# Optimization experiments

Measured on AMD Instinct MI355X. Metric: run time of the kernel, lower is better.

Reference implementation:

```python
import jax, jax.numpy as jnp
import numpy as np

B, S, F, E, R, O = 4, 2048, 2048, 16, 16, 2048
TEMPERATURE = 1.0


def setup_inputs() -> dict:
    key = jax.random.key(0)
    k1, k2, k3, k4 = jax.random.split(key, 4)
    x = jax.random.normal(k1, (B, S, F), dtype=jnp.float32)
    prototypes = jax.random.normal(k2, (E, F), dtype=jnp.float32)
    # prototypes are top right-singular vectors -> unit norm rows
    prototypes = prototypes / jnp.linalg.norm(prototypes, axis=1, keepdims=True)
    A_stack = jax.random.normal(k3, (E, R, F), dtype=jnp.float32) * 0.02
    B_stack = jax.random.normal(k4, (E, O, R), dtype=jnp.float32) * 0.02
    scaling = jnp.float32(2.0)
    return {"x": x, "prototypes": prototypes, "A_stack": A_stack,
            "B_stack": B_stack, "scaling": scaling, "top_k": 4}


def reference(x, prototypes, A_stack, B_stack, scaling, top_k):
    lead = x.shape[:-1]
    f_in = x.shape[-1]
    tok = x.reshape(-1, f_in)                       # (t, F)
    t = tok.shape[0]

    # Arrow routing: abs cosine-like similarity to per-expert prototypes
    sim = jnp.abs(tok @ prototypes.T)               # (t, E)
    top_v, idx = jax.lax.top_k(sim, top_k)          # (t, k)
    full_score = jnp.full(sim.shape, -jnp.inf, dtype=sim.dtype)
    full_score = full_score.at[jnp.arange(t)[:, None], idx].set(top_v)
    coeff = jax.nn.softmax(full_score / TEMPERATURE, axis=1)  # (t, E), zeros off top-k

    # Per-expert LoRA: z = tok @ A_e^T  (dense over all experts, as in source)
    z = jnp.einsum('tf,erf->ter', tok, A_stack)     # (t, E, r)
    # Combine coeff into the low-rank space before the B projection to avoid
    # materializing the (t, E, out) tensor; math identical to
    # einsum('te, teo -> to', coeff, einsum('ter,eor->teo', z, B_stack)).
    delta = jnp.einsum('te,ter,eor->to', coeff, z, B_stack)  # (t, O)

    delta = scaling * delta                          # dropout = identity (eval)
    return delta.reshape(lead + (delta.shape[-1],))
```

## Files before the change

### kernel.cpp

```cpp
#include <hip/hip_runtime.h>
#include <hip/hip_bf16.h>
#include <stdint.h>

#define T_TOKENS 8192
#define F_DIM    2048
#define E_EXP    16
#define R_RANK   16
#define O_DIM    2048
#define KDIM     (E_EXP * R_RANK)

typedef short v8s __attribute__((ext_vector_type(8)));
typedef float v4f __attribute__((ext_vector_type(4)));

#define AS1 __attribute__((address_space(1)))
#define AS3 __attribute__((address_space(3)))

__device__ __forceinline__ uint16_t f2bf(float f) {
  uint32_t u = __builtin_bit_cast(uint32_t, f);
  u += 0x7fffu + ((u >> 16) & 1u);
  return (uint16_t)(u >> 16);
}

__device__ __forceinline__ void g2lds16(const uint16_t* g, uint16_t* l) {
  __builtin_amdgcn_global_load_lds((AS1 void*)g, (AS3 void*)l, 16, 0, 0);
}

__global__ __launch_bounds__(256) void prep_weights(
    const float* __restrict__ A, const float* __restrict__ Bst,
    uint16_t* __restrict__ Ab, uint16_t* __restrict__ Bb) {
  int idx = blockIdx.x * 256 + threadIdx.x;
  if (idx < KDIM * F_DIM) {
    Ab[idx] = f2bf(A[idx]);
  }
  if (idx < O_DIM * KDIM) {
    int k = idx & (KDIM - 1);
    int o = idx >> 8;
    int e = k >> 4, r = k & 15;
    Bb[idx] = f2bf(Bst[((size_t)e * O_DIM + o) * R_RANK + r]);
  }
}

__global__ __launch_bounds__(256) void route_stream(
    const float* __restrict__ x, const float* __restrict__ P,
    uint16_t* __restrict__ xb, float4* __restrict__ partials4) {
  __shared__ float ps[16 * 260];
  const int tid = threadIdx.x;
  const int c   = blockIdx.x;
  const int by  = blockIdx.y;
  const int f0  = c * 256;

  {
    const int e = tid >> 4;
    #pragma unroll
    for (int j = 0; j < 4; ++j) {
      const int col = (tid & 15) * 4 + j * 64;
      *(float4*)&ps[e * 260 + col] =
          *(const float4*)&P[(size_t)e * F_DIM + f0 + col];
    }
  }
  __syncthreads();

  const int sub = tid & 15;
  const int tg  = tid >> 4;
  const int t0  = by * 64 + tg * 4;
  const float* xr = x + (size_t)t0 * F_DIM + f0;
  uint16_t*    xw = xb + (size_t)t0 * F_DIM + f0;

  float a0[16], a1[16], a2[16], a3[16];
  #pragma unroll
  for (int e = 0; e < 16; ++e) { a0[e] = 0.f; a1[e] = 0.f; a2[e] = 0.f; a3[e] = 0.f; }

  #pragma unroll
  for (int j = 0; j < 4; ++j) {
    const int off = sub * 4 + j * 64;
    float4 v0 = *(const float4*)&xr[off];
    float4 v1 = *(const float4*)&xr[F_DIM + off];
    float4 v2 = *(const float4*)&xr[2 * F_DIM + off];
    float4 v3 = *(const float4*)&xr[3 * F_DIM + off];
    uint2 p0, p1, p2, p3;
    p0.x = (uint32_t)f2bf(v0.x) | ((uint32_t)f2bf(v0.y) << 16);
    p0.y = (uint32_t)f2bf(v0.z) | ((uint32_t)f2bf(v0.w) << 16);
    p1.x = (uint32_t)f2bf(v1.x) | ((uint32_t)f2bf(v1.y) << 16);
    p1.y = (uint32_t)f2bf(v1.z) | ((uint32_t)f2bf(v1.w) << 16);
    p2.x = (uint32_t)f2bf(v2.x) | ((uint32_t)f2bf(v2.y) << 16);
    p2.y = (uint32_t)f2bf(v2.z) | ((uint32_t)f2bf(v2.w) << 16);
    p3.x = (uint32_t)f2bf(v3.x) | ((uint32_t)f2bf(v3.y) << 16);
    p3.y = (uint32_t)f2bf(v3.z) | ((uint32_t)f2bf(v3.w) << 16);
    *(uint2*)&xw[off]             = p0;
    *(uint2*)&xw[F_DIM + off]     = p1;
    *(uint2*)&xw[2 * F_DIM + off] = p2;
    *(uint2*)&xw[3 * F_DIM + off] = p3;
    #pragma unroll
    for (int e = 0; e < 16; ++e) {
      float4 pv = *(float4*)&ps[e * 260 + off];
      a0[e] += v0.x * pv.x; a0[e] += v0.y * pv.y; a0[e] += v0.z * pv.z; a0[e] += v0.w * pv.w;
      a1[e] += v1.x * pv.x; a1[e] += v1.y * pv.y; a1[e] += v1.z * pv.z; a1[e] += v1.w * pv.w;
      a2[e] += v2.x * pv.x; a2[e] += v2.y * pv.y; a2[e] += v2.z * pv.z; a2[e] += v2.w * pv.w;
      a3[e] += v3.x * pv.x; a3[e] += v3.y * pv.y; a3[e] += v3.z * pv.z; a3[e] += v3.w * pv.w;
    }
  }

  #pragma unroll
  for (int e = 0; e < 16; ++e) {
    #pragma unroll
    for (int m = 1; m < 16; m <<= 1) {
      a0[e] += __shfl_xor(a0[e], m, 64);
      a1[e] += __shfl_xor(a1[e], m, 64);
      a2[e] += __shfl_xor(a2[e], m, 64);
      a3[e] += __shfl_xor(a3[e], m, 64);
    }
  }

  const size_t cb = (size_t)c * 4;
  if (sub == 0) {
    #pragma unroll
    for (int e4 = 0; e4 < 4; ++e4)
      partials4[(cb + e4) * T_TOKENS + t0] =
          make_float4(a0[e4 * 4], a0[e4 * 4 + 1], a0[e4 * 4 + 2], a0[e4 * 4 + 3]);
  } else if (sub == 1) {
    #pragma unroll
    for (int e4 = 0; e4 < 4; ++e4)
      partials4[(cb + e4) * T_TOKENS + t0 + 1] =
          make_float4(a1[e4 * 4], a1[e4 * 4 + 1], a1[e4 * 4 + 2], a1[e4 * 4 + 3]);
  } else if (sub == 2) {
    #pragma unroll
    for (int e4 = 0; e4 < 4; ++e4)
      partials4[(cb + e4) * T_TOKENS + t0 + 2] =
          make_float4(a2[e4 * 4], a2[e4 * 4 + 1], a2[e4 * 4 + 2], a2[e4 * 4 + 3]);
  } else if (sub == 3) {
    #pragma unroll
    for (int e4 = 0; e4 < 4; ++e4)
      partials4[(cb + e4) * T_TOKENS + t0 + 3] =
          make_float4(a3[e4 * 4], a3[e4 * 4 + 1], a3[e4 * 4 + 2], a3[e4 * 4 + 3]);
  }
}

__global__ __launch_bounds__(256) void gemm_xa(
    const uint16_t* __restrict__ xb, const uint16_t* __restrict__ Ab,
    const float4* __restrict__ partials4, const float* __restrict__ scaling,
    const int* __restrict__ topk, uint16_t* __restrict__ wb) {
  __shared__ uint16_t S[16384];
  __shared__ float coeffL[64 * 17];
  uint16_t* Xh[2] = { S,         S + 4096  };
  uint16_t* Ah[2] = { S + 8192,  S + 12288 };
  const int tid  = threadIdx.x;
  const int b    = blockIdx.x;
  const int m_idx = (b & 7) + ((b >> 5) << 3);
  const int n_idx = (b >> 3) & 3;
  const int m0 = m_idx * 64, n0 = n_idx * 64;
  const int lane = tid & 63;
  const int wid  = tid >> 6;
  const int wm   = (wid >> 1) * 32;
  const int wn   = (wid & 1) * 32;
  const int quad = lane >> 4;
  const int cl   = lane & 15;

  if (tid < 64) {
    const int t = m0 + tid;
    double s[16];
    #pragma unroll
    for (int e = 0; e < 16; ++e) s[e] = 0.0;
    for (int c = 0; c < 8; ++c) {
      #pragma unroll
      for (int e4 = 0; e4 < 4; ++e4) {
        float4 p = partials4[((size_t)c * 4 + e4) * T_TOKENS + t];
        s[e4 * 4]     += (double)p.x;
        s[e4 * 4 + 1] += (double)p.y;
        s[e4 * 4 + 2] += (double)p.z;
        s[e4 * 4 + 3] += (double)p.w;
      }
    }
    double v[16];
    #pragma unroll
    for (int e = 0; e < 16; ++e) v[e] = fabs(s[e]);
    int k = topk[0];
    if (k > 16) k = 16;
    if (k < 1)  k = 1;
    unsigned mask = 0;
    double mx = 0.0;
    float ssum = 0.f;
    for (int i = 0; i < k; ++i) {
      double bv = -1.0; int bj = 0;
      #pragma unroll
      for (int j = 0; j < 16; ++j) {
        bool ok = !((mask >> j) & 1u) && (v[j] > bv);
        bv = ok ? v[j] : bv;
        bj = ok ? j  : bj;
      }
      mask |= 1u << bj;
      if (i == 0) mx = bv;
      ssum += expf((float)(bv - mx));
    }
    const float sc = scaling[0];
    #pragma unroll
    for (int j = 0; j < 16; ++j)
      coeffL[tid * 17 + j] = ((mask >> j) & 1u)
          ? expf((float)(v[j] - mx)) / ssum * sc : 0.f;
  }

  const int G0 = wid * 64 + lane;
  const int G1 = G0 + 256;
  const int r0 = G0 >> 3, g0 = (G0 & 7) ^ (r0 & 7);
  const int r1 = G1 >> 3, g1 = (G1 & 7) ^ (r1 & 7);
  const uint16_t* xs0 = xb + (size_t)(m0 + r0) * F_DIM + g0 * 8;
  const uint16_t* xs1 = xb + (size_t)(m0 + r1) * F_DIM + g1 * 8;
  const uint16_t* as0 = Ab + (size_t)(n0 + r0) * F_DIM + g0 * 8;
  const uint16_t* as1 = Ab + (size_t)(n0 + r1) * F_DIM + g1 * 8;
  const int d0 = wid * 512;
  const int d1 = wid * 512 + 2048;

  const int ma0 = wm + cl, ma1 = wm + 16 + cl;
  const int nb0 = wn + cl, nb1 = wn + 16 + cl;

  v4f acc[2][2];
  #pragma unroll
  for (int i = 0; i < 2; i++)
    #pragma unroll
    for (int j = 0; j < 2; j++) acc[i][j] = (v4f){0.f, 0.f, 0.f, 0.f};

  for (int k0 = 0; k0 < F_DIM; k0 += 128) {
    __syncthreads();
    g2lds16(xs0 + k0,      Xh[0] + d0);
    g2lds16(xs1 + k0,      Xh[0] + d1);
    g2lds16(as0 + k0,      Ah[0] + d0);
    g2lds16(as1 + k0,      Ah[0] + d1);
    g2lds16(xs0 + k0 + 64, Xh[1] + d0);
    g2lds16(xs1 + k0 + 64, Xh[1] + d1);
    g2lds16(as0 + k0 + 64, Ah[1] + d0);
    g2lds16(as1 + k0 + 64, Ah[1] + d1);
    __syncthreads();
    #pragma unroll
    for (int h = 0; h < 2; ++h) {
      #pragma unroll
      for (int ks = 0; ks < 2; ++ks) {
        const int gk = ks * 4 + quad;
        v8s fa0 = *(v8s*)&Xh[h][(ma0 * 8 + (gk ^ (ma0 & 7))) * 8];
        v8s fa1 = *(v8s*)&Xh[h][(ma1 * 8 + (gk ^ (ma1 & 7))) * 8];
        v8s fb0 = *(v8s*)&Ah[h][(nb0 * 8 + (gk ^ (nb0 & 7))) * 8];
        v8s fb1 = *(v8s*)&Ah[h][(nb1 * 8 + (gk ^ (nb1 & 7))) * 8];
        acc[0][0] = __builtin_amdgcn_mfma_f32_16x16x32_bf16(fa0, fb0, acc[0][0], 0, 0, 0);
        acc[0][1] = __builtin_amdgcn_mfma_f32_16x16x32_bf16(fa0, fb1, acc[0][1], 0, 0, 0);
        acc[1][0] = __builtin_amdgcn_mfma_f32_16x16x32_bf16(fa1, fb0, acc[1][0], 0, 0, 0);
        acc[1][1] = __builtin_amdgcn_mfma_f32_16x16x32_bf16(fa1, fb1, acc[1][1], 0, 0, 0);
      }
    }
  }

  __syncthreads();
  uint16_t* tile = S;
  #pragma unroll
  for (int mi = 0; mi < 2; mi++)
    #pragma unroll
    for (int ni = 0; ni < 2; ni++) {
      const int nl = wn + ni * 16 + cl;
      const int eidx = (n0 + nl) >> 4;
      #pragma unroll
      for (int reg = 0; reg < 4; reg++) {
        const int tl = wm + mi * 16 + quad * 4 + reg;
        float wv = acc[mi][ni][reg] * coeffL[tl * 17 + eidx];
        tile[tl * 72 + nl] = f2bf(wv);
      }
    }
  __syncthreads();
  #pragma unroll
  for (int p = 0; p < 2; ++p) {
    const int row  = p * 32 + (tid >> 3);
    const int colg = (tid & 7) * 8;
    uint4 val = *(uint4*)&tile[row * 72 + colg];
    *(uint4*)&wb[(size_t)(m0 + row) * KDIM + n0 + colg] = val;
  }
}

__global__ __launch_bounds__(256) void gemm_wb(
    const uint16_t* __restrict__ wbuf, const uint16_t* __restrict__ Bb,
    float* __restrict__ out) {
  __shared__ uint16_t S[20480];
  uint16_t* Ws = S;
  uint16_t* Bs = S + 4096;
  const int tid  = threadIdx.x;
  const int b    = blockIdx.x;
  const int m_idx = (b & 7) + ((b >> 6) << 3);
  const int n_idx = (b >> 3) & 7;
  const int m0 = m_idx * 64;
  const int n0 = n_idx * 256;
  const int lane = tid & 63;
  const int wid  = tid >> 6;
  const int wm   = (wid >> 1) * 32;
  const int wn   = (wid & 1) * 128;
  const int quad = lane >> 4;
  const int cl   = lane & 15;

  const int GW0 = wid * 64 + lane;
  const int GW1 = GW0 + 256;
  const int wr0 = GW0 >> 3, wg0 = (GW0 & 7) ^ (wr0 & 7);
  const int wr1 = GW1 >> 3, wg1 = (GW1 & 7) ^ (wr1 & 7);
  const uint16_t* wsrc0 = wbuf + (size_t)(m0 + wr0) * KDIM + wg0 * 8;
  const uint16_t* wsrc1 = wbuf + (size_t)(m0 + wr1) * KDIM + wg1 * 8;

  const uint16_t* bsrc[8];
  #pragma unroll
  for (int p = 0; p < 8; ++p) {
    const int G = p * 256 + wid * 64 + lane;
    const int r = G >> 3, g = (G & 7) ^ (r & 7);
    bsrc[p] = Bb + (size_t)(n0 + r) * KDIM + g * 8;
  }

  v4f acc[2][8];
  #pragma unroll
  for (int i = 0; i < 2; i++)
    #pragma unroll
    for (int j = 0; j < 8; j++) acc[i][j] = (v4f){0.f, 0.f, 0.f, 0.f};

  const int ma0 = wm + cl, ma1 = wm + 16 + cl;

  #pragma unroll
  for (int k0 = 0; k0 < KDIM; k0 += 64) {
    __syncthreads();
    g2lds16(wsrc0 + k0, Ws + wid * 512);
    g2lds16(wsrc1 + k0, Ws + wid * 512 + 2048);
    #pragma unroll
    for (int p = 0; p < 8; ++p)
      g2lds16(bsrc[p] + k0, Bs + (p * 256 + wid * 64) * 8);
    __syncthreads();
    #pragma unroll
    for (int ks = 0; ks < 2; ++ks) {
      const int gk = ks * 4 + quad;
      v8s fa0 = *(v8s*)&Ws[(ma0 * 8 + (gk ^ (ma0 & 7))) * 8];
      v8s fa1 = *(v8s*)&Ws[(ma1 * 8 + (gk ^ (ma1 & 7))) * 8];
      v8s fb[8];
      #pragma unroll
      for (int j = 0; j < 8; ++j) {
        const int nb = wn + j * 16 + cl;
        fb[j] = *(v8s*)&Bs[(nb * 8 + (gk ^ (nb & 7))) * 8];
      }
      #pragma unroll
      for (int j = 0; j < 8; ++j) {
        acc[0][j] = __builtin_amdgcn_mfma_f32_16x16x32_bf16(fa0, fb[j], acc[0][j], 0, 0, 0);
        acc[1][j] = __builtin_amdgcn_mfma_f32_16x16x32_bf16(fa1, fb[j], acc[1][j], 0, 0, 0);
      }
    }
  }

  float* ft = (float*)S;
  #pragma unroll
  for (int h = 0; h < 2; ++h) {
    __syncthreads();
    if ((wid >> 1) == h) {
      #pragma unroll
      for (int mi = 0; mi < 2; mi++)
        #pragma unroll
        for (int j = 0; j < 8; j++) {
          const int col = wn + j * 16 + cl;
          #pragma unroll
          for (int reg = 0; reg < 4; reg++) {
            const int rl = mi * 16 + quad * 4 + reg;
            ft[rl * 260 + col] = acc[mi][j][reg];
          }
        }
    }
    __syncthreads();
    #pragma unroll
    for (int p = 0; p < 8; ++p) {
      const int f4  = p * 256 + tid;
      const int row = f4 >> 6;
      const int c4  = f4 & 63;
      float4 v = *(float4*)&ft[row * 260 + c4 * 4];
      *(float4*)&out[(size_t)(m0 + h * 32 + row) * O_DIM + n0 + c4 * 4] = v;
    }
  }
}

extern "C" void kernel_launch(void* const* d_in, const int* in_sizes, int n_in,
                              void* d_out, int out_size, void* d_ws, size_t ws_size,
                              hipStream_t stream) {
  (void)in_sizes; (void)n_in; (void)out_size; (void)ws_size;
  const float* x       = (const float*)d_in[0];
  const float* P       = (const float*)d_in[1];
  const float* A       = (const float*)d_in[2];
  const float* Bst     = (const float*)d_in[3];
  const float* scaling = (const float*)d_in[4];
  const int*   topk    = (const int*)d_in[5];
  float* out = (float*)d_out;

  char* ws = (char*)d_ws;
  uint16_t* xb     = (uint16_t*)(ws);
  uint16_t* Ab     = (uint16_t*)(ws + 33554432);
  uint16_t* Bb     = (uint16_t*)(ws + 34603008);
  uint16_t* wbuf   = (uint16_t*)(ws + 35651584);
  float4*   parts  = (float4*)  (ws + 39845888);

  hipLaunchKernelGGL(prep_weights, dim3(2048), dim3(256), 0, stream, A, Bst, Ab, Bb);
  hipLaunchKernelGGL(route_stream, dim3(8, 128), dim3(256), 0, stream, x, P, xb, parts);
  hipLaunchKernelGGL(gemm_xa, dim3(512), dim3(256), 0, stream,
                     xb, Ab, parts, scaling, topk, wbuf);
  hipLaunchKernelGGL(gemm_wb, dim3(1024), dim3(256), 0, stream, wbuf, Bb, out);
}
```

Before: 167.0 us.

## Fuse weight prep into routing kernel and double-buffer XA GEMM loads

Removes the separate prep_weights launch by appending 64 extra blocks to route_stream that convert A and B to bf16. In gemm_xa, the coefficient computation now runs after the first LDS stage is issued, so its latency overlaps the load. The K loop becomes ping-pong double buffered so the next half-tile is fetched while the current one is multiplied. The aim is to cut launch overhead and hide global-to-LDS latency. The risks are that the few extra conversion blocks run as a tail in route_stream, and that synchronisation between stages becomes more intricate.

```diff
diff --git a/kernel.cpp b/kernel.cpp
--- a/kernel.cpp
+++ b/kernel.cpp
@@ -25,30 +25,30 @@
   __builtin_amdgcn_global_load_lds((AS1 void*)g, (AS3 void*)l, 16, 0, 0);
 }
 
-__global__ __launch_bounds__(256) void prep_weights(
-    const float* __restrict__ A, const float* __restrict__ Bst,
-    uint16_t* __restrict__ Ab, uint16_t* __restrict__ Bb) {
-  int idx = blockIdx.x * 256 + threadIdx.x;
-  if (idx < KDIM * F_DIM) {
-    Ab[idx] = f2bf(A[idx]);
-  }
-  if (idx < O_DIM * KDIM) {
-    int k = idx & (KDIM - 1);
-    int o = idx >> 8;
-    int e = k >> 4, r = k & 15;
-    Bb[idx] = f2bf(Bst[((size_t)e * O_DIM + o) * R_RANK + r]);
-  }
-}
-
 __global__ __launch_bounds__(256) void route_stream(
     const float* __restrict__ x, const float* __restrict__ P,
-    uint16_t* __restrict__ xb, float4* __restrict__ partials4) {
+    const float* __restrict__ A, const float* __restrict__ Bst,
+    uint16_t* __restrict__ xb, float4* __restrict__ partials4,
+    uint16_t* __restrict__ Ab, uint16_t* __restrict__ Bb) {
   __shared__ float ps[16 * 260];
   const int tid = threadIdx.x;
   const int c   = blockIdx.x;
   const int by  = blockIdx.y;
-  const int f0  = c * 256;
-
+
+  if (by >= 128) {
+    const int gid = ((by - 128) * 8 + c) * 256 + tid;
+    for (int i = gid; i < KDIM * F_DIM; i += 64 * 256)
+      Ab[i] = f2bf(A[i]);
+    for (int i = gid; i < O_DIM * KDIM; i += 64 * 256) {
+      const int k = i & (KDIM - 1);
+      const int o = i >> 8;
+      const int e = k >> 4, r = k & 15;
+      Bb[i] = f2bf(Bst[((size_t)e * O_DIM + o) * R_RANK + r]);
+    }
+    return;
+  }
+
+  const int f0 = c * 256;
   {
     const int e = tid >> 4;
     #pragma unroll
@@ -141,8 +141,10 @@
     const int* __restrict__ topk, uint16_t* __restrict__ wb) {
   __shared__ uint16_t S[16384];
   __shared__ float coeffL[64 * 17];
-  uint16_t* Xh[2] = { S,         S + 4096  };
-  uint16_t* Ah[2] = { S + 8192,  S + 12288 };
+  uint16_t* X0 = S;
+  uint16_t* X1 = S + 4096;
+  uint16_t* A0 = S + 8192;
+  uint16_t* A1 = S + 12288;
   const int tid  = threadIdx.x;
   const int b    = blockIdx.x;
   const int m_idx = (b & 7) + ((b >> 5) << 3);
@@ -155,49 +157,6 @@
   const int quad = lane >> 4;
   const int cl   = lane & 15;
 
-  if (tid < 64) {
-    const int t = m0 + tid;
-    double s[16];
-    #pragma unroll
-    for (int e = 0; e < 16; ++e) s[e] = 0.0;
-    for (int c = 0; c < 8; ++c) {
-      #pragma unroll
-      for (int e4 = 0; e4 < 4; ++e4) {
-        float4 p = partials4[((size_t)c * 4 + e4) * T_TOKENS + t];
-        s[e4 * 4]     += (double)p.x;
-        s[e4 * 4 + 1] += (double)p.y;
-        s[e4 * 4 + 2] += (double)p.z;
-        s[e4 * 4 + 3] += (double)p.w;
-      }
-    }
-    double v[16];
-    #pragma unroll
-    for (int e = 0; e < 16; ++e) v[e] = fabs(s[e]);
-    int k = topk[0];
-    if (k > 16) k = 16;
-    if (k < 1)  k = 1;
-    unsigned mask = 0;
-    double mx = 0.0;
-    float ssum = 0.f;
-    for (int i = 0; i < k; ++i) {
-      double bv = -1.0; int bj = 0;
-      #pragma unroll
-      for (int j = 0; j < 16; ++j) {
-        bool ok = !((mask >> j) & 1u) && (v[j] > bv);
-        bv = ok ? v[j] : bv;
-        bj = ok ? j  : bj;
-      }
-      mask |= 1u << bj;
-      if (i == 0) mx = bv;
-      ssum += expf((float)(bv - mx));
-    }
-    const float sc = scaling[0];
-    #pragma unroll
-    for (int j = 0; j < 16; ++j)
-      coeffL[tid * 17 + j] = ((mask >> j) & 1u)
-          ? expf((float)(v[j] - mx)) / ssum * sc : 0.f;
-  }
-
   const int G0 = wid * 64 + lane;
   const int G1 = G0 + 256;
   const int r0 = G0 >> 3, g0 = (G0 & 7) ^ (r0 & 7);
@@ -212,38 +171,86 @@
   const int ma0 = wm + cl, ma1 = wm + 16 + cl;
   const int nb0 = wn + cl, nb1 = wn + 16 + cl;
 
+#define STAGE_XA(Xb_, Ab_, kk) do {       \
+    g2lds16(xs0 + (kk), (Xb_) + d0);      \
+    g2lds16(xs1 + (kk), (Xb_) + d1);      \
+    g2lds16(as0 + (kk), (Ab_) + d0);      \
+    g2lds16(as1 + (kk), (Ab_) + d1);      \
+  } while (0)
+
+#define COMP_XA(Xb_, Ab_) do {                                                            \
+    _Pragma("unroll")                                                                     \
+    for (int ks = 0; ks < 2; ++ks) {                                                      \
+      const int gk = ks * 4 + quad;                                                       \
+      v8s fa0 = *(v8s*)&(Xb_)[(ma0 * 8 + (gk ^ (ma0 & 7))) * 8];                          \
+      v8s fa1 = *(v8s*)&(Xb_)[(ma1 * 8 + (gk ^ (ma1 & 7))) * 8];                          \
+      v8s fb0 = *(v8s*)&(Ab_)[(nb0 * 8 + (gk ^ (nb0 & 7))) * 8];                          \
+      v8s fb1 = *(v8s*)&(Ab_)[(nb1 * 8 + (gk ^ (nb1 & 7))) * 8];                          \
+      acc[0][0] = __builtin_amdgcn_mfma_f32_16x16x32_bf16(fa0, fb0, acc[0][0], 0, 0, 0);  \
+      acc[0][1] = __builtin_amdgcn_mfma_f32_16x16x32_bf16(fa0, fb1, acc[0][1], 0, 0, 0);  \
+      acc[1][0] = __builtin_amdgcn_mfma_f32_16x16x32_bf16(fa1, fb0, acc[1][0], 0, 0, 0);  \
+      acc[1][1] = __builtin_amdgcn_mfma_f32_16x16x32_bf16(fa1, fb1, acc[1][1], 0, 0, 0);  \
+    }                                                                                     \
+  } while (0)
+
   v4f acc[2][2];
   #pragma unroll
   for (int i = 0; i < 2; i++)
     #pragma unroll
     for (int j = 0; j < 2; j++) acc[i][j] = (v4f){0.f, 0.f, 0.f, 0.f};
 
+  STAGE_XA(X0, A0, 0);
+
+  if (tid < 64) {
+    const int t = m0 + tid;
+    double s[16];
+    #pragma unroll
+    for (int e = 0; e < 16; ++e) s[e] = 0.0;
+    for (int c = 0; c < 8; ++c) {
+      #pragma unroll
+      for (int e4 = 0; e4 < 4; ++e4) {
+        float4 p = partials4[((size_t)c * 4 + e4) * T_TOKENS + t];
+        s[e4 * 4]     += (double)p.x;
+        s[e4 * 4 + 1] += (double)p.y;
+        s[e4 * 4 + 2] += (double)p.z;
+        s[e4 * 4 + 3] += (double)p.w;
+      }
+    }
+    double v[16];
+    #pragma unroll
+    for (int e = 0; e < 16; ++e) v[e] = fabs(s[e]);
+    int k = topk[0];
+    if (k > 16) k = 16;
+    if (k < 1)  k = 1;
+    unsigned mask = 0;
+    double mx = 0.0;
+    float ssum = 0.f;
+    for (int i = 0; i < k; ++i) {
+      double bv = -1.0; int bj = 0;
+      #pragma unroll
+      for (int j = 0; j < 16; ++j) {
+        bool ok = !((mask >> j) & 1u) && (v[j] > bv);
+        bv = ok ? v[j] : bv;
+        bj = ok ? j  : bj;
+      }
+      mask |= 1u << bj;
+      if (i == 0) mx = bv;
+      ssum += expf((float)(bv - mx));
+    }
+    const float sc = scaling[0];
+    #pragma unroll
+    for (int j = 0; j < 16; ++j)
+      coeffL[tid * 17 + j] = ((mask >> j) & 1u)
+          ? expf((float)(v[j] - mx)) / ssum * sc : 0.f;
+  }
+
   for (int k0 = 0; k0 < F_DIM; k0 += 128) {
     __syncthreads();
-    g2lds16(xs0 + k0,      Xh[0] + d0);
-    g2lds16(xs1 + k0,      Xh[0] + d1);
-    g2lds16(as0 + k0,      Ah[0] + d0);
-    g2lds16(as1 + k0,      Ah[0] + d1);
-    g2lds16(xs0 + k0 + 64, Xh[1] + d0);
-    g2lds16(xs1 + k0 + 64, Xh[1] + d1);
-    g2lds16(as0 + k0 + 64, Ah[1] + d0);
-    g2lds16(as1 + k0 + 64, Ah[1] + d1);
-    __syncthreads();
-    #pragma unroll
-    for (int h = 0; h < 2; ++h) {
-      #pragma unroll
-      for (int ks = 0; ks < 2; ++ks) {
-        const int gk = ks * 4 + quad;
-        v8s fa0 = *(v8s*)&Xh[h][(ma0 * 8 + (gk ^ (ma0 & 7))) * 8];
-        v8s fa1 = *(v8s*)&Xh[h][(ma1 * 8 + (gk ^ (ma1 & 7))) * 8];
-        v8s fb0 = *(v8s*)&Ah[h][(nb0 * 8 + (gk ^ (nb0 & 7))) * 8];
-        v8s fb1 = *(v8s*)&Ah[h][(nb1 * 8 + (gk ^ (nb1 & 7))) * 8];
-        acc[0][0] = __builtin_amdgcn_mfma_f32_16x16x32_bf16(fa0, fb0, acc[0][0], 0, 0, 0);
-        acc[0][1] = __builtin_amdgcn_mfma_f32_16x16x32_bf16(fa0, fb1, acc[0][1], 0, 0, 0);
-        acc[1][0] = __builtin_amdgcn_mfma_f32_16x16x32_bf16(fa1, fb0, acc[1][0], 0, 0, 0);
-        acc[1][1] = __builtin_amdgcn_mfma_f32_16x16x32_bf16(fa1, fb1, acc[1][1], 0, 0, 0);
-      }
-    }
+    STAGE_XA(X1, A1, k0 + 64);
+    COMP_XA(X0, A0);
+    __syncthreads();
+    if (k0 + 128 < F_DIM) STAGE_XA(X0, A0, k0 + 128);
+    COMP_XA(X1, A1);
   }
 
   __syncthreads();
@@ -269,6 +276,8 @@
     uint4 val = *(uint4*)&tile[row * 72 + colg];
     *(uint4*)&wb[(size_t)(m0 + row) * KDIM + n0 + colg] = val;
   }
+#undef STAGE_XA
+#undef COMP_XA
 }
 
 __global__ __launch_bounds__(256) void gemm_wb(
@@ -389,8 +398,8 @@
   uint16_t* wbuf   = (uint16_t*)(ws + 35651584);
   float4*   parts  = (float4*)  (ws + 39845888);
 
-  hipLaunchKernelGGL(prep_weights, dim3(2048), dim3(256), 0, stream, A, Bst, Ab, Bb);
-  hipLaunchKernelGGL(route_stream, dim3(8, 128), dim3(256), 0, stream, x, P, xb, parts);
+  hipLaunchKernelGGL(route_stream, dim3(8, 136), dim3(256), 0, stream,
+                     x, P, A, Bst, xb, parts, Ab, Bb);
   hipLaunchKernelGGL(gemm_xa, dim3(512), dim3(256), 0, stream,
                      xb, Ab, parts, scaling, topk, wbuf);
   hipLaunchKernelGGL(gemm_wb, dim3(1024), dim3(256), 0, stream, wbuf, Bb, out);
```

Result: slower. 179.5 us (+7.5%).

## Fuse routing, bf16 conversion and x@A GEMM into one LDS-resident kernel

Applied to the files above, without the earlier changes.

Merges the routing/conversion kernel and the x@A GEMM into a single kernel where each block streams 32 token rows of fp32 x, computes prototype similarities, and stores bf16 x in LDS for the MFMA stage. This eliminates the global bf16 copy of x, the partial-sum buffer and one launch. Routing now sums in fp32 instead of double, and the large LDS footprint limits each CU to one block with less latency hiding.

```diff
diff --git a/kernel.cpp b/kernel.cpp
--- a/kernel.cpp
+++ b/kernel.cpp
@@ -21,8 +21,8 @@
   return (uint16_t)(u >> 16);
 }
 
-__device__ __forceinline__ void g2lds16(const uint16_t* g, uint16_t* l) {
-  __builtin_amdgcn_global_load_lds((AS1 void*)g, (AS3 void*)l, 16, 0, 0);
+__device__ __forceinline__ void g2lds16(const void* g, void* l) {
+  __builtin_amdgcn_global_load_lds((const AS1 void*)g, (AS3 void*)l, 16, 0, 0);
 }
 
 __global__ __launch_bounds__(256) void prep_weights(
@@ -40,234 +40,158 @@
   }
 }
 
-__global__ __launch_bounds__(256) void route_stream(
+__global__ __launch_bounds__(256) void fused_xa(
     const float* __restrict__ x, const float* __restrict__ P,
-    uint16_t* __restrict__ xb, float4* __restrict__ partials4) {
-  __shared__ float ps[16 * 260];
-  const int tid = threadIdx.x;
-  const int c   = blockIdx.x;
-  const int by  = blockIdx.y;
-  const int f0  = c * 256;
-
-  {
-    const int e = tid >> 4;
-    #pragma unroll
-    for (int j = 0; j < 4; ++j) {
-      const int col = (tid & 15) * 4 + j * 64;
-      *(float4*)&ps[e * 260 + col] =
-          *(const float4*)&P[(size_t)e * F_DIM + f0 + col];
-    }
-  }
-  __syncthreads();
-
-  const int sub = tid & 15;
-  const int tg  = tid >> 4;
-  const int t0  = by * 64 + tg * 4;
-  const float* xr = x + (size_t)t0 * F_DIM + f0;
-  uint16_t*    xw = xb + (size_t)t0 * F_DIM + f0;
-
-  float a0[16], a1[16], a2[16], a3[16];
-  #pragma unroll
-  for (int e = 0; e < 16; ++e) { a0[e] = 0.f; a1[e] = 0.f; a2[e] = 0.f; a3[e] = 0.f; }
-
-  #pragma unroll
-  for (int j = 0; j < 4; ++j) {
-    const int off = sub * 4 + j * 64;
-    float4 v0 = *(const float4*)&xr[off];
-    float4 v1 = *(const float4*)&xr[F_DIM + off];
-    float4 v2 = *(const float4*)&xr[2 * F_DIM + off];
-    float4 v3 = *(const float4*)&xr[3 * F_DIM + off];
-    uint2 p0, p1, p2, p3;
-    p0.x = (uint32_t)f2bf(v0.x) | ((uint32_t)f2bf(v0.y) << 16);
-    p0.y = (uint32_t)f2bf(v0.z) | ((uint32_t)f2bf(v0.w) << 16);
-    p1.x = (uint32_t)f2bf(v1.x) | ((uint32_t)f2bf(v1.y) << 16);
-    p1.y = (uint32_t)f2bf(v1.z) | ((uint32_t)f2bf(v1.w) << 16);
-    p2.x = (uint32_t)f2bf(v2.x) | ((uint32_t)f2bf(v2.y) << 16);
-    p2.y = (uint32_t)f2bf(v2.z) | ((uint32_t)f2bf(v2.w) << 16);
-    p3.x = (uint32_t)f2bf(v3.x) | ((uint32_t)f2bf(v3.y) << 16);
-    p3.y = (uint32_t)f2bf(v3.z) | ((uint32_t)f2bf(v3.w) << 16);
-    *(uint2*)&xw[off]             = p0;
-    *(uint2*)&xw[F_DIM + off]     = p1;
-    *(uint2*)&xw[2 * F_DIM + off] = p2;
-    *(uint2*)&xw[3 * F_DIM + off] = p3;
-    #pragma unroll
-    for (int e = 0; e < 16; ++e) {
-      float4 pv = *(float4*)&ps[e * 260 + off];
-      a0[e] += v0.x * pv.x; a0[e] += v0.y * pv.y; a0[e] += v0.z * pv.z; a0[e] += v0.w * pv.w;
-      a1[e] += v1.x * pv.x; a1[e] += v1.y * pv.y; a1[e] += v1.z * pv.z; a1[e] += v1.w * pv.w;
-      a2[e] += v2.x * pv.x; a2[e] += v2.y * pv.y; a2[e] += v2.z * pv.z; a2[e] += v2.w * pv.w;
-      a3[e] += v3.x * pv.x; a3[e] += v3.y * pv.y; a3[e] += v3.z * pv.z; a3[e] += v3.w * pv.w;
-    }
-  }
-
-  #pragma unroll
-  for (int e = 0; e < 16; ++e) {
-    #pragma unroll
-    for (int m = 1; m < 16; m <<= 1) {
-      a0[e] += __shfl_xor(a0[e], m, 64);
-      a1[e] += __shfl_xor(a1[e], m, 64);
-      a2[e] += __shfl_xor(a2[e], m, 64);
-      a3[e] += __shfl_xor(a3[e], m, 64);
-    }
-  }
-
-  const size_t cb = (size_t)c * 4;
-  if (sub == 0) {
-    #pragma unroll
-    for (int e4 = 0; e4 < 4; ++e4)
-      partials4[(cb + e4) * T_TOKENS + t0] =
-          make_float4(a0[e4 * 4], a0[e4 * 4 + 1], a0[e4 * 4 + 2], a0[e4 * 4 + 3]);
-  } else if (sub == 1) {
-    #pragma unroll
-    for (int e4 = 0; e4 < 4; ++e4)
-      partials4[(cb + e4) * T_TOKENS + t0 + 1] =
-          make_float4(a1[e4 * 4], a1[e4 * 4 + 1], a1[e4 * 4 + 2], a1[e4 * 4 + 3]);
-  } else if (sub == 2) {
-    #pragma unroll
-    for (int e4 = 0; e4 < 4; ++e4)
-      partials4[(cb + e4) * T_TOKENS + t0 + 2] =
-          make_float4(a2[e4 * 4], a2[e4 * 4 + 1], a2[e4 * 4 + 2], a2[e4 * 4 + 3]);
-  } else if (sub == 3) {
-    #pragma unroll
-    for (int e4 = 0; e4 < 4; ++e4)
-      partials4[(cb + e4) * T_TOKENS + t0 + 3] =
-          make_float4(a3[e4 * 4], a3[e4 * 4 + 1], a3[e4 * 4 + 2], a3[e4 * 4 + 3]);
-  }
-}
-
-__global__ __launch_bounds__(256) void gemm_xa(
-    const uint16_t* __restrict__ xb, const uint16_t* __restrict__ Ab,
-    const float4* __restrict__ partials4, const float* __restrict__ scaling,
+    const uint16_t* __restrict__ Ab, const float* __restrict__ scaling,
     const int* __restrict__ topk, uint16_t* __restrict__ wb) {
-  __shared__ uint16_t S[16384];
-  __shared__ float coeffL[64 * 17];
-  uint16_t* Xh[2] = { S,         S + 4096  };
-  uint16_t* Ah[2] = { S + 8192,  S + 12288 };
+  __shared__ uint16_t SH[75072];
+  uint16_t* xbf   = SH;
+  float*    Pl    = (float*)(SH + 65536);
+  uint16_t* tile  = SH + 65536;
+  float*    coeffL= (float*)((char*)SH + 131072 + 16896);
+
   const int tid  = threadIdx.x;
-  const int b    = blockIdx.x;
-  const int m_idx = (b & 7) + ((b >> 5) << 3);
-  const int n_idx = (b >> 3) & 3;
-  const int m0 = m_idx * 64, n0 = n_idx * 64;
+  const int m0   = blockIdx.x * 32;
   const int lane = tid & 63;
   const int wid  = tid >> 6;
-  const int wm   = (wid >> 1) * 32;
-  const int wn   = (wid & 1) * 32;
   const int quad = lane >> 4;
   const int cl   = lane & 15;
-
-  if (tid < 64) {
-    const int t = m0 + tid;
-    double s[16];
-    #pragma unroll
-    for (int e = 0; e < 16; ++e) s[e] = 0.0;
-    for (int c = 0; c < 8; ++c) {
-      #pragma unroll
-      for (int e4 = 0; e4 < 4; ++e4) {
-        float4 p = partials4[((size_t)c * 4 + e4) * T_TOKENS + t];
-        s[e4 * 4]     += (double)p.x;
-        s[e4 * 4 + 1] += (double)p.y;
-        s[e4 * 4 + 2] += (double)p.z;
-        s[e4 * 4 + 3] += (double)p.w;
-      }
-    }
-    double v[16];
-    #pragma unroll
-    for (int e = 0; e < 16; ++e) v[e] = fabs(s[e]);
-    int k = topk[0];
-    if (k > 16) k = 16;
-    if (k < 1)  k = 1;
-    unsigned mask = 0;
-    double mx = 0.0;
-    float ssum = 0.f;
-    for (int i = 0; i < k; ++i) {
-      double bv = -1.0; int bj = 0;
-      #pragma unroll
-      for (int j = 0; j < 16; ++j) {
-        bool ok = !((mask >> j) & 1u) && (v[j] > bv);
-        bv = ok ? v[j] : bv;
-        bj = ok ? j  : bj;
-      }
-      mask |= 1u << bj;
-      if (i == 0) mx = bv;
-      ssum += expf((float)(bv - mx));
-    }
+  const int tg   = tid >> 4;
+  const int slot = tid & 15;
+
+  float part0[16], part1[16];
+  #pragma unroll
+  for (int e = 0; e < 16; ++e) { part0[e] = 0.f; part1[e] = 0.f; }
+
+  const float* xr0 = x + (size_t)(m0 + tg) * F_DIM;
+  const float* xr1 = x + (size_t)(m0 + tg + 16) * F_DIM;
+  const int half  = slot & 1;
+  const int r0x   = tg & 7;
+
+  for (int ch = 0; ch < 8; ++ch) {
+    const int c0 = ch * 256;
+    #pragma unroll
+    for (int p = 0; p < 4; ++p) {
+      const int G = p * 256 + tid;
+      g2lds16(&P[(size_t)(G >> 6) * F_DIM + c0 + (G & 63) * 4],
+              (char*)Pl + (p * 256 + wid * 64) * 16);
+    }
+    __syncthreads();
+
+    #pragma unroll
+    for (int s = 0; s < 4; ++s) {
+      const int off = c0 + s * 64 + slot * 4;
+      float4 xv0 = *(const float4*)&xr0[off];
+      float4 xv1 = *(const float4*)&xr1[off];
+      const int gcol = off >> 3;
+      const int sl   = (gcol & ~7) | ((gcol & 7) ^ r0x);
+      uint2 pk0, pk1;
+      pk0.x = (uint32_t)f2bf(xv0.x) | ((uint32_t)f2bf(xv0.y) << 16);
+      pk0.y = (uint32_t)f2bf(xv0.z) | ((uint32_t)f2bf(xv0.w) << 16);
+      pk1.x = (uint32_t)f2bf(xv1.x) | ((uint32_t)f2bf(xv1.y) << 16);
+      pk1.y = (uint32_t)f2bf(xv1.z) | ((uint32_t)f2bf(xv1.w) << 16);
+      *(uint2*)((char*)xbf + (size_t)tg * 4096 + sl * 16 + half * 8)        = pk0;
+      *(uint2*)((char*)xbf + (size_t)(tg + 16) * 4096 + sl * 16 + half * 8) = pk1;
+      #pragma unroll
+      for (int e = 0; e < 16; ++e) {
+        float4 pv = *(float4*)&Pl[e * 256 + s * 64 + slot * 4];
+        part0[e] += xv0.x * pv.x; part0[e] += xv0.y * pv.y;
+        part0[e] += xv0.z * pv.z; part0[e] += xv0.w * pv.w;
+        part1[e] += xv1.x * pv.x; part1[e] += xv1.y * pv.y;
+        part1[e] += xv1.z * pv.z; part1[e] += xv1.w * pv.w;
+      }
+    }
+    __syncthreads();
+  }
+
+  #pragma unroll
+  for (int m = 1; m <= 8; m <<= 1) {
+    #pragma unroll
+    for (int e = 0; e < 16; ++e) {
+      part0[e] += __shfl_xor(part0[e], m, 64);
+      part1[e] += __shfl_xor(part1[e], m, 64);
+    }
+  }
+  {
+    int kk = topk[0];
+    if (kk > 16) kk = 16;
+    if (kk < 1)  kk = 1;
     const float sc = scaling[0];
     #pragma unroll
-    for (int j = 0; j < 16; ++j)
-      coeffL[tid * 17 + j] = ((mask >> j) & 1u)
-          ? expf((float)(v[j] - mx)) / ssum * sc : 0.f;
-  }
-
-  const int G0 = wid * 64 + lane;
-  const int G1 = G0 + 256;
-  const int r0 = G0 >> 3, g0 = (G0 & 7) ^ (r0 & 7);
-  const int r1 = G1 >> 3, g1 = (G1 & 7) ^ (r1 & 7);
-  const uint16_t* xs0 = xb + (size_t)(m0 + r0) * F_DIM + g0 * 8;
-  const uint16_t* xs1 = xb + (size_t)(m0 + r1) * F_DIM + g1 * 8;
-  const uint16_t* as0 = Ab + (size_t)(n0 + r0) * F_DIM + g0 * 8;
-  const uint16_t* as1 = Ab + (size_t)(n0 + r1) * F_DIM + g1 * 8;
-  const int d0 = wid * 512;
-  const int d1 = wid * 512 + 2048;
-
-  const int ma0 = wm + cl, ma1 = wm + 16 + cl;
-  const int nb0 = wn + cl, nb1 = wn + 16 + cl;
-
-  v4f acc[2][2];
+    for (int h = 0; h < 2; ++h) {
+      float v[16];
+      #pragma unroll
+      for (int e = 0; e < 16; ++e) v[e] = fabsf(h ? part1[e] : part0[e]);
+      unsigned mask = 0;
+      float mx = 0.f, ssum = 0.f;
+      for (int i = 0; i < kk; ++i) {
+        float bv = -1.f; int bj = 0;
+        #pragma unroll
+        for (int j = 0; j < 16; ++j) {
+          bool ok = !((mask >> j) & 1u) && (v[j] > bv);
+          bv = ok ? v[j] : bv;
+          bj = ok ? j   : bj;
+        }
+        mask |= 1u << bj;
+        if (i == 0) mx = bv;
+        ssum += expf(bv - mx);
+      }
+      coeffL[(tg + h * 16) * 17 + slot] = ((mask >> slot) & 1u)
+          ? expf(v[slot] - mx) / ssum * sc : 0.f;
+    }
+  }
+  __syncthreads();
+
+  v4f acc[2][4];
   #pragma unroll
   for (int i = 0; i < 2; i++)
     #pragma unroll
-    for (int j = 0; j < 2; j++) acc[i][j] = (v4f){0.f, 0.f, 0.f, 0.f};
-
-  for (int k0 = 0; k0 < F_DIM; k0 += 128) {
-    __syncthreads();
-    g2lds16(xs0 + k0,      Xh[0] + d0);
-    g2lds16(xs1 + k0,      Xh[0] + d1);
-    g2lds16(as0 + k0,      Ah[0] + d0);
-    g2lds16(as1 + k0,      Ah[0] + d1);
-    g2lds16(xs0 + k0 + 64, Xh[1] + d0);
-    g2lds16(xs1 + k0 + 64, Xh[1] + d1);
-    g2lds16(as0 + k0 + 64, Ah[1] + d0);
-    g2lds16(as1 + k0 + 64, Ah[1] + d1);
-    __syncthreads();
-    #pragma unroll
-    for (int h = 0; h < 2; ++h) {
-      #pragma unroll
-      for (int ks = 0; ks < 2; ++ks) {
-        const int gk = ks * 4 + quad;
-        v8s fa0 = *(v8s*)&Xh[h][(ma0 * 8 + (gk ^ (ma0 & 7))) * 8];
-        v8s fa1 = *(v8s*)&Xh[h][(ma1 * 8 + (gk ^ (ma1 & 7))) * 8];
-        v8s fb0 = *(v8s*)&Ah[h][(nb0 * 8 + (gk ^ (nb0 & 7))) * 8];
-        v8s fb1 = *(v8s*)&Ah[h][(nb1 * 8 + (gk ^ (nb1 & 7))) * 8];
-        acc[0][0] = __builtin_amdgcn_mfma_f32_16x16x32_bf16(fa0, fb0, acc[0][0], 0, 0, 0);
-        acc[0][1] = __builtin_amdgcn_mfma_f32_16x16x32_bf16(fa0, fb1, acc[0][1], 0, 0, 0);
-        acc[1][0] = __builtin_amdgcn_mfma_f32_16x16x32_bf16(fa1, fb0, acc[1][0], 0, 0, 0);
-        acc[1][1] = __builtin_amdgcn_mfma_f32_16x16x32_bf16(fa1, fb1, acc[1][1], 0, 0, 0);
-      }
-    }
-  }
-
+    for (int j = 0; j < 4; j++) acc[i][j] = (v4f){0.f, 0.f, 0.f, 0.f};
+
+  const uint16_t* Ap[4];
+  #pragma unroll
+  for (int j = 0; j < 4; ++j) {
+    const int nb = wid * 64 + j * 16 + cl;
+    Ap[j] = Ab + (size_t)nb * F_DIM + quad * 8;
+  }
+  const char* fa0p = (char*)xbf + (size_t)cl * 4096;
+  const char* fa1p = fa0p + 16 * 4096;
+  const int   clx  = cl & 7;
+
+  #pragma unroll 4
+  for (int s = 0; s < 64; ++s) {
+    const int g  = s * 4 + quad;
+    const int sl = (g & ~7) | ((g & 7) ^ clx);
+    v8s fa0 = *(const v8s*)(fa0p + sl * 16);
+    v8s fa1 = *(const v8s*)(fa1p + sl * 16);
+    #pragma unroll
+    for (int j = 0; j < 4; ++j) {
+      v8s fb = *(const v8s*)(Ap[j] + s * 32);
+      acc[0][j] = __builtin_amdgcn_mfma_f32_16x16x32_bf16(fa0, fb, acc[0][j], 0, 0, 0);
+      acc[1][j] = __builtin_amdgcn_mfma_f32_16x16x32_bf16(fa1, fb, acc[1][j], 0, 0, 0);
+    }
+  }
+
+  #pragma unroll
+  for (int mi = 0; mi < 2; ++mi)
+    #pragma unroll
+    for (int j = 0; j < 4; ++j) {
+      const int col = wid * 64 + j * 16 + cl;
+      const int e   = wid * 4 + j;
+      #pragma unroll
+      for (int reg = 0; reg < 4; ++reg) {
+        const int tl = mi * 16 + quad * 4 + reg;
+        tile[tl * 264 + col] = f2bf(acc[mi][j][reg] * coeffL[tl * 17 + e]);
+      }
+    }
   __syncthreads();
-  uint16_t* tile = S;
-  #pragma unroll
-  for (int mi = 0; mi < 2; mi++)
-    #pragma unroll
-    for (int ni = 0; ni < 2; ni++) {
-      const int nl = wn + ni * 16 + cl;
-      const int eidx = (n0 + nl) >> 4;
-      #pragma unroll
-      for (int reg = 0; reg < 4; reg++) {
-        const int tl = wm + mi * 16 + quad * 4 + reg;
-        float wv = acc[mi][ni][reg] * coeffL[tl * 17 + eidx];
-        tile[tl * 72 + nl] = f2bf(wv);
-      }
-    }
-  __syncthreads();
-  #pragma unroll
-  for (int p = 0; p < 2; ++p) {
-    const int row  = p * 32 + (tid >> 3);
-    const int colg = (tid & 7) * 8;
-    uint4 val = *(uint4*)&tile[row * 72 + colg];
-    *(uint4*)&wb[(size_t)(m0 + row) * KDIM + n0 + colg] = val;
+  #pragma unroll
+  for (int p = 0; p < 4; ++p) {
+    const int f4  = p * 256 + tid;
+    const int row = f4 >> 5;
+    const int c16 = f4 & 31;
+    *(uint4*)&wb[(size_t)(m0 + row) * KDIM + c16 * 8] =
+        *(uint4*)&tile[row * 264 + c16 * 8];
   }
 }
 
@@ -383,15 +307,12 @@
   float* out = (float*)d_out;
 
   char* ws = (char*)d_ws;
-  uint16_t* xb     = (uint16_t*)(ws);
-  uint16_t* Ab     = (uint16_t*)(ws + 33554432);
-  uint16_t* Bb     = (uint16_t*)(ws + 34603008);
-  uint16_t* wbuf   = (uint16_t*)(ws + 35651584);
-  float4*   parts  = (float4*)  (ws + 39845888);
+  uint16_t* Ab   = (uint16_t*)(ws);
+  uint16_t* Bb   = (uint16_t*)(ws + 1048576);
+  uint16_t* wbuf = (uint16_t*)(ws + 2097152);
 
   hipLaunchKernelGGL(prep_weights, dim3(2048), dim3(256), 0, stream, A, Bst, Ab, Bb);
-  hipLaunchKernelGGL(route_stream, dim3(8, 128), dim3(256), 0, stream, x, P, xb, parts);
-  hipLaunchKernelGGL(gemm_xa, dim3(512), dim3(256), 0, stream,
-                     xb, Ab, parts, scaling, topk, wbuf);
+  hipLaunchKernelGGL(fused_xa, dim3(256), dim3(256), 0, stream,
+                     x, P, Ab, scaling, topk, wbuf);
   hipLaunchKernelGGL(gemm_wb, dim3(1024), dim3(256), 0, stream, wbuf, Bb, out);
 }
```

Measured after the change: 201.8 us. 1.21x slower.

## Restructure routing kernel: one row per 8 threads, direct-to-LDS prototype load

Applied to the files above, without the earlier changes.

The routing/bf16-conversion kernel now gives each group of 8 threads one token row, loading all eight float4s up front, instead of 16 threads handling 4 rows. This cuts register pressure (16 accumulators instead of 64) and the shuffle-reduction depth, and doubles the grid so more blocks are in flight. Prototypes are copied into LDS with global_load_lds, dropping the padded layout. The unpadded LDS layout may add bank conflicts on the prototype reads.

```diff
diff --git a/kernel.cpp b/kernel.cpp
--- a/kernel.cpp
+++ b/kernel.cpp
@@ -21,8 +21,8 @@
   return (uint16_t)(u >> 16);
 }
 
-__device__ __forceinline__ void g2lds16(const uint16_t* g, uint16_t* l) {
-  __builtin_amdgcn_global_load_lds((AS1 void*)g, (AS3 void*)l, 16, 0, 0);
+__device__ __forceinline__ void g2lds16(const void* g, void* l) {
+  __builtin_amdgcn_global_load_lds((const AS1 void*)g, (AS3 void*)l, 16, 0, 0);
 }
 
 __global__ __launch_bounds__(256) void prep_weights(
@@ -43,95 +43,64 @@
 __global__ __launch_bounds__(256) void route_stream(
     const float* __restrict__ x, const float* __restrict__ P,
     uint16_t* __restrict__ xb, float4* __restrict__ partials4) {
-  __shared__ float ps[16 * 260];
+  __shared__ float ps[16 * 256];
   const int tid = threadIdx.x;
   const int c   = blockIdx.x;
   const int by  = blockIdx.y;
   const int f0  = c * 256;
 
-  {
-    const int e = tid >> 4;
-    #pragma unroll
-    for (int j = 0; j < 4; ++j) {
-      const int col = (tid & 15) * 4 + j * 64;
-      *(float4*)&ps[e * 260 + col] =
-          *(const float4*)&P[(size_t)e * F_DIM + f0 + col];
-    }
+  #pragma unroll
+  for (int p = 0; p < 4; ++p) {
+    const int G = p * 256 + tid;
+    g2lds16(&P[(size_t)(G >> 6) * F_DIM + f0 + (G & 63) * 4],
+            (char*)ps + (p * 256 + (tid >> 6) * 64) * 16);
   }
   __syncthreads();
 
-  const int sub = tid & 15;
-  const int tg  = tid >> 4;
-  const int t0  = by * 64 + tg * 4;
-  const float* xr = x + (size_t)t0 * F_DIM + f0;
-  uint16_t*    xw = xb + (size_t)t0 * F_DIM + f0;
-
-  float a0[16], a1[16], a2[16], a3[16];
-  #pragma unroll
-  for (int e = 0; e < 16; ++e) { a0[e] = 0.f; a1[e] = 0.f; a2[e] = 0.f; a3[e] = 0.f; }
-
-  #pragma unroll
-  for (int j = 0; j < 4; ++j) {
-    const int off = sub * 4 + j * 64;
-    float4 v0 = *(const float4*)&xr[off];
-    float4 v1 = *(const float4*)&xr[F_DIM + off];
-    float4 v2 = *(const float4*)&xr[2 * F_DIM + off];
-    float4 v3 = *(const float4*)&xr[3 * F_DIM + off];
-    uint2 p0, p1, p2, p3;
-    p0.x = (uint32_t)f2bf(v0.x) | ((uint32_t)f2bf(v0.y) << 16);
-    p0.y = (uint32_t)f2bf(v0.z) | ((uint32_t)f2bf(v0.w) << 16);
-    p1.x = (uint32_t)f2bf(v1.x) | ((uint32_t)f2bf(v1.y) << 16);
-    p1.y = (uint32_t)f2bf(v1.z) | ((uint32_t)f2bf(v1.w) << 16);
-    p2.x = (uint32_t)f2bf(v2.x) | ((uint32_t)f2bf(v2.y) << 16);
-    p2.y = (uint32_t)f2bf(v2.z) | ((uint32_t)f2bf(v2.w) << 16);
-    p3.x = (uint32_t)f2bf(v3.x) | ((uint32_t)f2bf(v3.y) << 16);
-    p3.y = (uint32_t)f2bf(v3.z) | ((uint32_t)f2bf(v3.w) << 16);
-    *(uint2*)&xw[off]             = p0;
-    *(uint2*)&xw[F_DIM + off]     = p1;
-    *(uint2*)&xw[2 * F_DIM + off] = p2;
-    *(uint2*)&xw[3 * F_DIM + off] = p3;
+  const int sub = tid & 7;
+  const int tg  = tid >> 3;
+  const int row = by * 32 + tg;
+  const float* xr = x  + (size_t)row * F_DIM + f0;
+  uint16_t*    xw = xb + (size_t)row * F_DIM + f0;
+
+  float a[16];
+  #pragma unroll
+  for (int e = 0; e < 16; ++e) a[e] = 0.f;
+
+  float4 v[8];
+  #pragma unroll
+  for (int k = 0; k < 8; ++k)
+    v[k] = *(const float4*)&xr[sub * 4 + k * 32];
+
+  #pragma unroll
+  for (int k = 0; k < 8; ++k) {
+    uint2 pk;
+    pk.x = (uint32_t)f2bf(v[k].x) | ((uint32_t)f2bf(v[k].y) << 16);
+    pk.y = (uint32_t)f2bf(v[k].z) | ((uint32_t)f2bf(v[k].w) << 16);
+    *(uint2*)&xw[sub * 4 + k * 32] = pk;
+  }
+
+  #pragma unroll
+  for (int k = 0; k < 8; ++k) {
+    const int col = sub * 4 + k * 32;
     #pragma unroll
     for (int e = 0; e < 16; ++e) {
-      float4 pv = *(float4*)&ps[e * 260 + off];
-      a0[e] += v0.x * pv.x; a0[e] += v0.y * pv.y; a0[e] += v0.z * pv.z; a0[e] += v0.w * pv.w;
-      a1[e] += v1.x * pv.x; a1[e] += v1.y * pv.y; a1[e] += v1.z * pv.z; a1[e] += v1.w * pv.w;
-      a2[e] += v2.x * pv.x; a2[e] += v2.y * pv.y; a2[e] += v2.z * pv.z; a2[e] += v2.w * pv.w;
-      a3[e] += v3.x * pv.x; a3[e] += v3.y * pv.y; a3[e] += v3.z * pv.z; a3[e] += v3.w * pv.w;
-    }
-  }
-
-  #pragma unroll
-  for (int e = 0; e < 16; ++e) {
-    #pragma unroll
-    for (int m = 1; m < 16; m <<= 1) {
-      a0[e] += __shfl_xor(a0[e], m, 64);
-      a1[e] += __shfl_xor(a1[e], m, 64);
-      a2[e] += __shfl_xor(a2[e], m, 64);
-      a3[e] += __shfl_xor(a3[e], m, 64);
-    }
-  }
-
-  const size_t cb = (size_t)c * 4;
-  if (sub == 0) {
-    #pragma unroll
-    for (int e4 = 0; e4 < 4; ++e4)
-      partials4[(cb + e4) * T_TOKENS + t0] =
-          make_float4(a0[e4 * 4], a0[e4 * 4 + 1], a0[e4 * 4 + 2], a0[e4 * 4 + 3]);
-  } else if (sub == 1) {
-    #pragma unroll
-    for (int e4 = 0; e4 < 4; ++e4)
-      partials4[(cb + e4) * T_TOKENS + t0 + 1] =
-          make_float4(a1[e4 * 4], a1[e4 * 4 + 1], a1[e4 * 4 + 2], a1[e4 * 4 + 3]);
-  } else if (sub == 2) {
-    #pragma unroll
-    for (int e4 = 0; e4 < 4; ++e4)
-      partials4[(cb + e4) * T_TOKENS + t0 + 2] =
-          make_float4(a2[e4 * 4], a2[e4 * 4 + 1], a2[e4 * 4 + 2], a2[e4 * 4 + 3]);
-  } else if (sub == 3) {
-    #pragma unroll
-    for (int e4 = 0; e4 < 4; ++e4)
-      partials4[(cb + e4) * T_TOKENS + t0 + 3] =
-          make_float4(a3[e4 * 4], a3[e4 * 4 + 1], a3[e4 * 4 + 2], a3[e4 * 4 + 3]);
+      float4 pv = *(float4*)&ps[e * 256 + col];
+      a[e] += v[k].x * pv.x; a[e] += v[k].y * pv.y;
+      a[e] += v[k].z * pv.z; a[e] += v[k].w * pv.w;
+    }
+  }
+
+  #pragma unroll
+  for (int m = 1; m <= 4; m <<= 1) {
+    #pragma unroll
+    for (int e = 0; e < 16; ++e)
+      a[e] += __shfl_xor(a[e], m, 64);
+  }
+
+  if (sub < 4) {
+    partials4[((size_t)c * 4 + sub) * T_TOKENS + row] =
+        make_float4(a[sub * 4], a[sub * 4 + 1], a[sub * 4 + 2], a[sub * 4 + 3]);
   }
 }
 
@@ -390,7 +359,7 @@
   float4*   parts  = (float4*)  (ws + 39845888);
 
   hipLaunchKernelGGL(prep_weights, dim3(2048), dim3(256), 0, stream, A, Bst, Ab, Bb);
-  hipLaunchKernelGGL(route_stream, dim3(8, 128), dim3(256), 0, stream, x, P, xb, parts);
+  hipLaunchKernelGGL(route_stream, dim3(8, 256), dim3(256), 0, stream, x, P, xb, parts);
   hipLaunchKernelGGL(gemm_xa, dim3(512), dim3(256), 0, stream,
                      xb, Ab, parts, scaling, topk, wbuf);
   hipLaunchKernelGGL(gemm_wb, dim3(1024), dim3(256), 0, stream, wbuf, Bb, out);
```

New measurement: 165.4 us. No clear change (-1.0%).
